# Optimization experiments

Measured on AMD Instinct MI355X. Metric: run time of the kernel, lower is better.

Reference implementation:

```python
import jax, jax.numpy as jnp
import numpy as np
import math

B, T, H, L, N = 8, 256, 1024, 6, 16
S = 3 * T          # interleaved (rtg, state, action) tokens
D = H // N
STATE_DIM, ACT_DIM, MAX_TSTEP, FF = 1024, 64, 4096, 4 * H
EPS = 1e-5


def _ln(x, g, b):
    m = jnp.mean(x, axis=-1, keepdims=True)
    v = jnp.var(x, axis=-1, keepdims=True)
    return (x - m) * jax.lax.rsqrt(v + EPS) * g + b


def setup_inputs() -> dict:
    key = jax.random.key(0)
    ks = jax.random.split(key, 32)
    sc = 0.02
    inp = {
        'timesteps': jax.random.randint(ks[0], (B, T), 0, MAX_TSTEP),
        'states': jax.random.randint(ks[1], (B, T), 0, STATE_DIM),
        'actions': jax.random.randint(ks[2], (B, T), 0, ACT_DIM),
        'returns_to_go': jax.random.normal(ks[3], (B, T, 1), jnp.float32),
        # embeddings
        'Wt': jax.random.normal(ks[4], (MAX_TSTEP, H), jnp.float32) * sc,
        'Ws': jax.random.normal(ks[5], (STATE_DIM, H), jnp.float32) * sc,
        'Wa': jax.random.normal(ks[6], (ACT_DIM, H), jnp.float32) * sc,
        'Wr': jax.random.normal(ks[7], (1, H), jnp.float32) * sc,
        'br': jnp.zeros((H,), jnp.float32),
        'lng': jnp.ones((H,), jnp.float32), 'lnb': jnp.zeros((H,), jnp.float32),
        # per-layer stacked params (weights stored [in,out]: y = x @ W + b)
        'Wq': jax.random.normal(ks[8], (L, H, H), jnp.float32) * sc,
        'bq': jnp.zeros((L, H), jnp.float32),
        'Wk': jax.random.normal(ks[9], (L, H, H), jnp.float32) * sc,
        'bk': jnp.zeros((L, H), jnp.float32),
        'Wv': jax.random.normal(ks[10], (L, H, H), jnp.float32) * sc,
        'bv': jnp.zeros((L, H), jnp.float32),
        'Wp': jax.random.normal(ks[11], (L, H, H), jnp.float32) * sc,
        'bp': jnp.zeros((L, H), jnp.float32),
        'W1': jax.random.normal(ks[12], (L, H, FF), jnp.float32) * sc,
        'b1': jnp.zeros((L, FF), jnp.float32),
        'W2': jax.random.normal(ks[13], (L, FF, H), jnp.float32) * sc,
        'b2': jnp.zeros((L, H), jnp.float32),
        'ln1g': jnp.ones((L, H), jnp.float32), 'ln1b': jnp.zeros((L, H), jnp.float32),
        'ln2g': jnp.ones((L, H), jnp.float32), 'ln2b': jnp.zeros((L, H), jnp.float32),
        # heads
        'Wrtg': jax.random.normal(ks[14], (H, 1), jnp.float32) * sc,
        'brtg': jnp.zeros((1,), jnp.float32),
        'Wst': jax.random.normal(ks[15], (H, STATE_DIM), jnp.float32) * sc,
        'bst': jnp.zeros((STATE_DIM,), jnp.float32),
        'Wac': jax.random.normal(ks[16], (H, ACT_DIM), jnp.float32) * sc,
        'bac': jnp.zeros((ACT_DIM,), jnp.float32),
    }
    return inp


def _attn(x, Wq, bq, Wk, bk, Wv, bv, Wp, bp, mask):
    q = (x @ Wq + bq).reshape(B, S, N, D)
    k = (x @ Wk + bk).reshape(B, S, N, D)
    v = (x @ Wv + bv).reshape(B, S, N, D)
    scores = jnp.einsum('bqhd,bkhd->bhqk', q, k) / math.sqrt(D)
    scores = jnp.where(mask, scores, -jnp.inf)
    p = jax.nn.softmax(scores, axis=-1)
    o = jnp.einsum('bhqk,bkhd->bqhd', p, v).reshape(B, S, H)
    return o @ Wp + bp


def _forward(timesteps, states, actions, returns_to_go, Wt, Ws, Wa, Wr, br,
             lng, lnb, Wq, bq, Wk, bk, Wv, bv, Wp, bp, W1, b1, W2, b2,
             ln1g, ln1b, ln2g, ln2b, Wrtg, brtg, Wst, bst, Wac, bac):
    te = Wt[timesteps]                         # [B,T,H]
    se = Ws[states] + te
    ae = Wa[actions] + te
    re = returns_to_go @ Wr + br + te
    # stack(dim=1).permute(0,2,1,3).reshape -> interleave (rtg, state, action)
    h = jnp.stack([re, se, ae], axis=2).reshape(B, S, H)
    h = _ln(h, lng, lnb)
    mask = jnp.tril(jnp.ones((S, S), bool))[None, None]
    for l in range(L):
        h = h + _attn(h, Wq[l], bq[l], Wk[l], bk[l], Wv[l], bv[l], Wp[l], bp[l], mask)
        h = _ln(h, ln1g[l], ln1b[l])
        h = h + (jax.nn.gelu(h @ W1[l] + b1[l], approximate=False) @ W2[l] + b2[l])
        h = _ln(h, ln2g[l], ln2b[l])
    h = h.reshape(B, 3, T, H)                  # as in the source (contiguous chunks)
    rtg_preds = h[:, 2] @ Wrtg + brtg
    state_preds = h[:, 2] @ Wst + bst
    action_preds = h[:, 1] @ Wac + bac         # discrete actions -> no tanh
    return (state_preds, action_preds, rtg_preds)


def reference(timesteps, states, actions, returns_to_go, Wt, Ws, Wa, Wr, br,
              lng, lnb, Wq, bq, Wk, bk, Wv, bv, Wp, bp, W1, b1, W2, b2,
              ln1g, ln1b, ln2g, ln2b, Wrtg, brtg, Wst, bst, Wac, bac):
    return _forward(timesteps, states, actions, returns_to_go, Wt, Ws, Wa, Wr, br,
                    lng, lnb, Wq, bq, Wk, bk, Wv, bv, Wp, bp, W1, b1, W2, b2,
                    ln1g, ln1b, ln2g, ln2b, Wrtg, brtg, Wst, bst, Wac, bac)
```

## Files before the change

### kernel.cpp

```cpp
#include <hip/hip_runtime.h>
#include <hip/hip_bf16.h>

#define DI __device__ __forceinline__

typedef unsigned short u16;
typedef __bf16 bf16x8 __attribute__((ext_vector_type(8)));
typedef unsigned short u16x8 __attribute__((ext_vector_type(8)));
typedef unsigned short u16x4 __attribute__((ext_vector_type(4)));
typedef float f32x4 __attribute__((ext_vector_type(4)));

static constexpr int Bb = 8, Tt = 256, Hh = 1024, Ll = 6, NHd = 16, Dh = 64;
static constexpr int Ss = 3 * Tt;
static constexpr int FFd = 4096;
static constexpr int BSr = Bb * Ss;
static constexpr int QKVld = 3072;

DI u16 f2bf(float f) {
  unsigned u = __builtin_bit_cast(unsigned, f);
  u += 0x7fffu + ((u >> 16) & 1u);
  return (u16)(u >> 16);
}

DI void gload_lds16(const u16* g, u16* l) {
  __builtin_amdgcn_global_load_lds((__attribute__((address_space(1))) void*)(g),
                                   (__attribute__((address_space(3))) void*)(l), 16, 0, 0);
}
DI bf16x8 ldl8(const u16* p) { return __builtin_bit_cast(bf16x8, *(const u16x8*)p); }
DI bf16x8 ldg8(const u16* p) { return __builtin_bit_cast(bf16x8, *(const u16x8*)p); }

DI void barRaw() {
  asm volatile("" ::: "memory");
  __builtin_amdgcn_s_barrier();
  asm volatile("" ::: "memory");
}

__global__ __launch_bounds__(256, 4) void gemm_db(
    const u16* __restrict__ A, const u16* __restrict__ Bt,
    const float* __restrict__ bias, const float* __restrict__ bias2,
    const float* __restrict__ bias3,
    float* __restrict__ outf, u16* __restrict__ outb,
    int Kstride, int Ksub, int ldc, int act, size_t psz)
{
  __shared__ u16 LA[3][128 * 32];
  __shared__ u16 LB[3][128 * 32];
  const int lane = threadIdx.x & 63, w = threadIdx.x >> 6;
  const int wr = w >> 1, wc = w & 1;
  const int l15 = lane & 15, l4 = lane >> 4;

  const int gx = gridDim.x, nwg = gx * gridDim.y;
  int f = blockIdx.y * gx + blockIdx.x;
  { int q = nwg >> 3, rr = nwg & 7, x = f & 7, idx = f >> 3;
    f = (x < rr ? x * (q + 1) : rr * (q + 1) + (x - rr) * q) + idx; }
  const int bm = f / gx, bn = f % gx;
  const int koff = blockIdx.z * Ksub;
  const int NT = Ksub >> 5;

  const int srow = lane >> 2;
  const int schunk = (((lane & 3) ^ ((srow >> 1) & 3)) << 3);
  unsigned aoff[2], boff[2];
#pragma unroll
  for (int i = 0; i < 2; ++i) {
    const int r = w * 32 + i * 16 + srow;
    aoff[i] = (unsigned)(bm * 128 + r) * (unsigned)Kstride + koff + schunk;
    boff[i] = (unsigned)(bn * 128 + r) * (unsigned)Kstride + koff + schunk;
  }

  auto stage = [&](int bsel, int kt) {
#pragma unroll
    for (int i = 0; i < 2; ++i) {
      gload_lds16(A + aoff[i] + kt * 32, &LA[bsel][(w * 32 + i * 16) * 32]);
      gload_lds16(Bt + boff[i] + kt * 32, &LB[bsel][(w * 32 + i * 16) * 32]);
    }
  };

  f32x4 acc[4][4] = {};

  stage(0, 0);
  stage(1, 1);
  asm volatile("s_waitcnt vmcnt(4)" ::: "memory");
  barRaw();

  const int ck = ((l4 ^ ((l15 >> 1) & 3)) << 3);
  int cur = 0;
  for (int t = 0; t < NT; ++t) {
    const int nxt = (cur + 2 >= 3) ? cur - 1 : cur + 2;
    if (t + 2 < NT) stage(nxt, t + 2);

    bf16x8 af[4], bf[4];
#pragma unroll
    for (int m = 0; m < 4; ++m)
      af[m] = ldl8(&LA[cur][(wr * 64 + m * 16 + l15) * 32 + ck]);
#pragma unroll
    for (int n = 0; n < 4; ++n)
      bf[n] = ldl8(&LB[cur][(wc * 64 + n * 16 + l15) * 32 + ck]);

    __builtin_amdgcn_s_setprio(1);
#pragma unroll
    for (int m = 0; m < 4; ++m)
#pragma unroll
      for (int n = 0; n < 4; ++n)
        acc[m][n] = __builtin_amdgcn_mfma_f32_16x16x32_bf16(af[m], bf[n], acc[m][n], 0, 0, 0);
    __builtin_amdgcn_s_setprio(0);

    if (t + 2 < NT)      asm volatile("s_waitcnt vmcnt(4)" ::: "memory");
    else if (t + 1 < NT) asm volatile("s_waitcnt vmcnt(0)" ::: "memory");
    barRaw();
    cur = (cur + 1 >= 3) ? 0 : cur + 1;
  }

#pragma unroll
  for (int n = 0; n < 4; ++n) {
    const int col = bn * 128 + wc * 64 + n * 16 + l15;
    float bval = 0.f;
    if (bias) {
      const float* bp_ = bias;
      int idx = col;
      if (bias2 && col >= 1024) { bp_ = (col >= 2048) ? bias3 : bias2; idx = col & 1023; }
      bval = bp_[idx];
    }
#pragma unroll
    for (int m = 0; m < 4; ++m) {
#pragma unroll
      for (int r = 0; r < 4; ++r) {
        const int row = bm * 128 + wr * 64 + m * 16 + l4 * 4 + r;
        float x = acc[m][n][r] + bval;
        if (act) x = 0.5f * x * (1.f + erff(x * 0.70710678118654752f));
        if (outf) outf[blockIdx.z * psz + (size_t)row * ldc + col] = x;
        if (outb) outb[(size_t)row * ldc + col] = f2bf(x);
      }
    }
  }
}

__global__ __launch_bounds__(256, 2) void gemm_bf16(
    const u16* __restrict__ A, const u16* __restrict__ Bt,
    const float* __restrict__ bias, float* __restrict__ outf,
    int M, int N, int K, int ldc, int Nstore, int rowmode, int rowoff)
{
  __shared__ u16 As[128 * 64];
  __shared__ u16 Bs[128 * 64];
  const int tid = threadIdx.x;
  const int lane = tid & 63;
  const int w = tid >> 6;
  const int wr = w >> 1, wc = w & 1;
  const int bn = blockIdx.x, bm = blockIdx.y;
  const int l3 = lane >> 3, l7 = lane & 7, l15 = lane & 15, l4 = lane >> 4;

  f32x4 acc[4][4] = {};

  const int schunk = (l7 ^ l3) << 3;
  size_t aoff[4], boff[4];
#pragma unroll
  for (int i = 0; i < 4; ++i) {
    int r = bm * 128 + w * 32 + i * 8 + l3;
    int ar = rowmode ? ((r >> 8) * Ss + rowoff + (r & 255)) : r;
    aoff[i] = (size_t)ar * K + schunk;
    boff[i] = (size_t)(bn * 128 + w * 32 + i * 8 + l3) * K + schunk;
  }

  for (int kt = 0; kt < K; kt += 64) {
    __syncthreads();
#pragma unroll
    for (int i = 0; i < 4; ++i) {
      gload_lds16(A + aoff[i] + kt, &As[(w * 32 + i * 8) * 64]);
      gload_lds16(Bt + boff[i] + kt, &Bs[(w * 32 + i * 8) * 64]);
    }
    __syncthreads();

    bf16x8 af[4][2], bf[4][2];
#pragma unroll
    for (int m = 0; m < 4; ++m) {
#pragma unroll
      for (int kk = 0; kk < 2; ++kk) {
        const int slot = ((kk * 4 + l4) ^ l7) << 3;
        af[m][kk] = ldl8(&As[(wr * 64 + m * 16 + l15) * 64 + slot]);
        bf[m][kk] = ldl8(&Bs[(wc * 64 + m * 16 + l15) * 64 + slot]);
      }
    }
#pragma unroll
    for (int m = 0; m < 4; ++m)
#pragma unroll
      for (int n = 0; n < 4; ++n)
#pragma unroll
        for (int kk = 0; kk < 2; ++kk)
          acc[m][n] = __builtin_amdgcn_mfma_f32_16x16x32_bf16(af[m][kk], bf[n][kk], acc[m][n], 0, 0, 0);
  }

#pragma unroll
  for (int n = 0; n < 4; ++n) {
    const int col = bn * 128 + wc * 64 + n * 16 + l15;
    const bool cok = col < Nstore;
    const float bv = (cok && bias) ? bias[col] : 0.f;
#pragma unroll
    for (int m = 0; m < 4; ++m) {
#pragma unroll
      for (int r = 0; r < 4; ++r) {
        const int row = bm * 128 + wr * 64 + m * 16 + l4 * 4 + r;
        if (cok) outf[(size_t)row * ldc + col] = acc[m][n][r] + bv;
      }
    }
  }
}

__global__ __launch_bounds__(256, 3) void attn_flash(
    const u16* __restrict__ qkv, const u16* __restrict__ vt, u16* __restrict__ o)
{
  __shared__ u16 Kl[2][64 * 64];
  __shared__ u16 Vl[2][64 * 64];
  __shared__ u16 Pl[4][16 * 64];
  const int qt = blockIdx.x, h = blockIdx.y, b = blockIdx.z;
  const int lane = threadIdx.x & 63, w = threadIdx.x >> 6;
  const int l15 = lane & 15, l4 = lane >> 4;

  const size_t qoff = (size_t)(b * Ss + qt * 64 + w * 16 + l15) * QKVld + h * Dh + l4 * 8;
  const bf16x8 aq0 = ldg8(qkv + qoff), aq1 = ldg8(qkv + qoff + 32);

  const u16* kg = qkv + (size_t)b * Ss * QKVld + 1024 + h * Dh;
  const u16* vg = vt + (size_t)(b * NHd + h) * Dh * Ss;

  int srow[2], scs[2];
#pragma unroll
  for (int i = 0; i < 2; ++i) {
    srow[i] = (w * 2 + i) * 8 + (lane >> 3);
    scs[i] = ((lane & 7) ^ (srow[i] & 7)) * 8;
  }

  float m[4] = {-1e30f, -1e30f, -1e30f, -1e30f};
  float lsum[4] = {0.f, 0.f, 0.f, 0.f};
  f32x4 oa[4] = {};

  auto stage = [&](int bsel, int kb) {
#pragma unroll
    for (int i = 0; i < 2; ++i) {
      gload_lds16(kg + (size_t)(kb * 64 + srow[i]) * QKVld + scs[i], &Kl[bsel][(w * 2 + i) * 8 * 64]);
      gload_lds16(vg + (size_t)srow[i] * Ss + kb * 64 + scs[i], &Vl[bsel][(w * 2 + i) * 8 * 64]);
    }
  };

  stage(0, 0);
  __syncthreads();
  int buf = 0;
  for (int kb = 0; kb <= qt; ++kb) {
    if (kb < qt) stage(buf ^ 1, kb + 1);

    f32x4 sc[4];
    __builtin_amdgcn_s_setprio(1);
#pragma unroll
    for (int fj = 0; fj < 4; ++fj) {
      const u16* kp = &Kl[buf][(fj * 16 + l15) * 64];
      const int r7 = l15 & 7;
      bf16x8 kf0 = ldl8(kp + ((l4 ^ r7) << 3));
      bf16x8 kf1 = ldl8(kp + (((4 + l4) ^ r7) << 3));
      f32x4 zz = {};
      zz = __builtin_amdgcn_mfma_f32_16x16x32_bf16(aq0, kf0, zz, 0, 0, 0);
      sc[fj] = __builtin_amdgcn_mfma_f32_16x16x32_bf16(aq1, kf1, zz, 0, 0, 0);
    }
    __builtin_amdgcn_s_setprio(0);

    float pm[4] = {-1e30f, -1e30f, -1e30f, -1e30f};
    const bool diag = (kb == qt);
#pragma unroll
    for (int fj = 0; fj < 4; ++fj)
#pragma unroll
      for (int r = 0; r < 4; ++r) {
        float s = sc[fj][r] * 0.125f;
        if (diag && (fj * 16 + l15) > (w * 16 + l4 * 4 + r)) s = -1e30f;
        sc[fj][r] = s;
        pm[r] = fmaxf(pm[r], s);
      }
#pragma unroll
    for (int d = 1; d < 16; d <<= 1)
#pragma unroll
      for (int r = 0; r < 4; ++r) pm[r] = fmaxf(pm[r], __shfl_xor(pm[r], d));

    float al[4], ps[4];
#pragma unroll
    for (int r = 0; r < 4; ++r) {
      float mn = fmaxf(m[r], pm[r]);
      al[r] = __expf(m[r] - mn);
      m[r] = mn;
      ps[r] = 0.f;
    }
#pragma unroll
    for (int fj = 0; fj < 4; ++fj)
#pragma unroll
      for (int r = 0; r < 4; ++r) {
        float p = __expf(sc[fj][r] - m[r]);
        sc[fj][r] = p;
        ps[r] += p;
      }
#pragma unroll
    for (int d = 1; d < 16; d <<= 1)
#pragma unroll
      for (int r = 0; r < 4; ++r) ps[r] += __shfl_xor(ps[r], d);
#pragma unroll
    for (int r = 0; r < 4; ++r) lsum[r] = lsum[r] * al[r] + ps[r];
#pragma unroll
    for (int fn = 0; fn < 4; ++fn)
#pragma unroll
      for (int r = 0; r < 4; ++r) oa[fn][r] *= al[r];

#pragma unroll
    for (int fj = 0; fj < 4; ++fj)
#pragma unroll
      for (int r = 0; r < 4; ++r) {
        const int key = fj * 16 + l15, qloc = l4 * 4 + r;
        Pl[w][qloc * 64 + (((key >> 3) ^ (qloc & 7)) << 3) + (key & 7)] = f2bf(sc[fj][r]);
      }

    const int q7 = l15 & 7;
    bf16x8 pa0 = ldl8(&Pl[w][l15 * 64 + ((l4 ^ q7) << 3)]);
    bf16x8 pa1 = ldl8(&Pl[w][l15 * 64 + (((4 + l4) ^ q7) << 3)]);
    __builtin_amdgcn_s_setprio(1);
#pragma unroll
    for (int fn = 0; fn < 4; ++fn) {
      const u16* vp = &Vl[buf][(fn * 16 + l15) * 64];
      bf16x8 vf0 = ldl8(vp + ((l4 ^ q7) << 3));
      bf16x8 vf1 = ldl8(vp + (((4 + l4) ^ q7) << 3));
      oa[fn] = __builtin_amdgcn_mfma_f32_16x16x32_bf16(pa0, vf0, oa[fn], 0, 0, 0);
      oa[fn] = __builtin_amdgcn_mfma_f32_16x16x32_bf16(pa1, vf1, oa[fn], 0, 0, 0);
    }
    __builtin_amdgcn_s_setprio(0);
    __syncthreads();
    buf ^= 1;
  }

#pragma unroll
  for (int fn = 0; fn < 4; ++fn)
#pragma unroll
    for (int r = 0; r < 4; ++r) {
      const int row = b * Ss + qt * 64 + w * 16 + l4 * 4 + r;
      o[(size_t)row * Hh + h * Dh + fn * 16 + l15] = f2bf(oa[fn][r] / lsum[r]);
    }
}

__global__ __launch_bounds__(256) void embed_ln(
    const int* __restrict__ timesteps, const int* __restrict__ states,
    const int* __restrict__ actions, const float* __restrict__ rtg,
    const float* __restrict__ Wt, const float* __restrict__ Ws,
    const float* __restrict__ Wa, const float* __restrict__ Wr,
    const float* __restrict__ br, const float* __restrict__ lng,
    const float* __restrict__ lnb, float* __restrict__ hout, u16* __restrict__ xb)
{
  __shared__ float red[8];
  const int s = blockIdx.x;
  const int b = s / Ss, sl = s % Ss;
  const int tt = sl / 3, kind = sl % 3;
  const int bt = b * Tt + tt;
  const int e = threadIdx.x * 4;

  const float4 tv = *(const float4*)(Wt + (size_t)timesteps[bt] * Hh + e);
  float v[4];
  if (kind == 0) {
    const float rr = rtg[bt];
    const float4 w4 = *(const float4*)(Wr + e);
    const float4 b4 = *(const float4*)(br + e);
    v[0] = rr * w4.x + b4.x + tv.x; v[1] = rr * w4.y + b4.y + tv.y;
    v[2] = rr * w4.z + b4.z + tv.z; v[3] = rr * w4.w + b4.w + tv.w;
  } else {
    const float* emb = (kind == 1) ? (Ws + (size_t)states[bt] * Hh)
                                   : (Wa + (size_t)actions[bt] * Hh);
    const float4 e4 = *(const float4*)(emb + e);
    v[0] = e4.x + tv.x; v[1] = e4.y + tv.y; v[2] = e4.z + tv.z; v[3] = e4.w + tv.w;
  }
  float s1 = v[0] + v[1] + v[2] + v[3];
  float s2 = v[0]*v[0] + v[1]*v[1] + v[2]*v[2] + v[3]*v[3];
#pragma unroll
  for (int d = 32; d; d >>= 1) { s1 += __shfl_xor(s1, d); s2 += __shfl_xor(s2, d); }
  if ((threadIdx.x & 63) == 0) { red[threadIdx.x >> 6] = s1; red[4 + (threadIdx.x >> 6)] = s2; }
  __syncthreads();
  s1 = red[0] + red[1] + red[2] + red[3];
  s2 = red[4] + red[5] + red[6] + red[7];
  const float mean = s1 * (1.f / 1024.f);
  const float var = s2 * (1.f / 1024.f) - mean * mean;
  const float rs = rsqrtf(var + 1e-5f);
  const float4 g4 = *(const float4*)(lng + e);
  const float4 bb4 = *(const float4*)(lnb + e);
  float o0 = (v[0] - mean) * rs * g4.x + bb4.x;
  float o1 = (v[1] - mean) * rs * g4.y + bb4.y;
  float o2 = (v[2] - mean) * rs * g4.z + bb4.z;
  float o3 = (v[3] - mean) * rs * g4.w + bb4.w;
  *(float4*)(hout + (size_t)s * Hh + e) = make_float4(o0, o1, o2, o3);
  u16x4 ov = {f2bf(o0), f2bf(o1), f2bf(o2), f2bf(o3)};
  *(u16x4*)(xb + (size_t)s * Hh + e) = ov;
}

__global__ __launch_bounds__(256) void ln_kernel(
    const float* __restrict__ inA, const float* __restrict__ inB,
    const float* __restrict__ resid, const float* __restrict__ bias,
    const float* __restrict__ g, const float* __restrict__ bta,
    float* __restrict__ hout, u16* __restrict__ xb)
{
  __shared__ float red[8];
  const int row = blockIdx.x;
  const int e = threadIdx.x * 4;
  const float4 a4 = *(const float4*)(inA + (size_t)row * Hh + e);
  float v[4] = {a4.x, a4.y, a4.z, a4.w};
  if (inB) {
    const float4 b4 = *(const float4*)(inB + (size_t)row * Hh + e);
    v[0] += b4.x; v[1] += b4.y; v[2] += b4.z; v[3] += b4.w;
  }
  if (resid) {
    const float4 r4 = *(const float4*)(resid + (size_t)row * Hh + e);
    v[0] += r4.x; v[1] += r4.y; v[2] += r4.z; v[3] += r4.w;
  }
  if (bias) {
    const float4 c4 = *(const float4*)(bias + e);
    v[0] += c4.x; v[1] += c4.y; v[2] += c4.z; v[3] += c4.w;
  }
  float s1 = v[0] + v[1] + v[2] + v[3];
  float s2 = v[0]*v[0] + v[1]*v[1] + v[2]*v[2] + v[3]*v[3];
#pragma unroll
  for (int d = 32; d; d >>= 1) { s1 += __shfl_xor(s1, d); s2 += __shfl_xor(s2, d); }
  if ((threadIdx.x & 63) == 0) { red[threadIdx.x >> 6] = s1; red[4 + (threadIdx.x >> 6)] = s2; }
  __syncthreads();
  s1 = red[0] + red[1] + red[2] + red[3];
  s2 = red[4] + red[5] + red[6] + red[7];
  const float mean = s1 * (1.f / 1024.f);
  const float var = s2 * (1.f / 1024.f) - mean * mean;
  const float rs = rsqrtf(var + 1e-5f);
  const float4 g4 = *(const float4*)(g + e);
  const float4 b4 = *(const float4*)(bta + e);
  float o0 = (v[0] - mean) * rs * g4.x + b4.x;
  float o1 = (v[1] - mean) * rs * g4.y + b4.y;
  float o2 = (v[2] - mean) * rs * g4.z + b4.z;
  float o3 = (v[3] - mean) * rs * g4.w + b4.w;
  *(float4*)(hout + (size_t)row * Hh + e) = make_float4(o0, o1, o2, o3);
  u16x4 ov = {f2bf(o0), f2bf(o1), f2bf(o2), f2bf(o3)};
  *(u16x4*)(xb + (size_t)row * Hh + e) = ov;
}

__global__ __launch_bounds__(256) void transpose_w(
    const float* __restrict__ W, u16* __restrict__ Wt, int Kd, int Nd, int Nout)
{
  __shared__ float tile[32][33];
  const int k0 = blockIdx.x * 32, n0 = blockIdx.y * 32;
  const int tx = threadIdx.x & 31, ty = threadIdx.x >> 5;
#pragma unroll
  for (int rr = 0; rr < 4; ++rr) {
    const int kk = ty + rr * 8;
    const int n = n0 + tx;
    tile[kk][tx] = (n < Nd) ? W[(size_t)(k0 + kk) * Nd + n] : 0.f;
  }
  __syncthreads();
#pragma unroll
  for (int rr = 0; rr < 4; ++rr) {
    Wt[(size_t)(n0 + ty + rr * 8) * Kd + k0 + tx] = f2bf(tile[tx][ty + rr * 8]);
  }
}

__global__ __launch_bounds__(256) void transpose_v(
    const u16* __restrict__ v, u16* __restrict__ vt)
{
  __shared__ u16 tile[64][72];
  const int s0 = blockIdx.x * 64, h = blockIdx.y, b = blockIdx.z;
  const int j8 = (threadIdx.x & 7) * 8;
#pragma unroll
  for (int half = 0; half < 2; ++half) {
    const int i = (threadIdx.x >> 3) + half * 32;
    *(u16x8*)&tile[i][j8] =
        *(const u16x8*)&v[(size_t)(b * Ss + s0 + i) * QKVld + 2048 + h * 64 + j8];
  }
  __syncthreads();
#pragma unroll
  for (int half = 0; half < 2; ++half) {
    const int d = (threadIdx.x >> 3) + half * 32;
    u16x8 ov;
#pragma unroll
    for (int ee = 0; ee < 8; ++ee) ov[ee] = tile[j8 + ee][d];
    *(u16x8*)&vt[((size_t)(b * NHd + h) * 64 + d) * Ss + s0 + j8] = ov;
  }
}

__global__ __launch_bounds__(256) void rtg_head(
    const float* __restrict__ h, const float* __restrict__ Wr1,
    const float* __restrict__ br1, float* __restrict__ out)
{
  const int lane = threadIdx.x & 63, w = threadIdx.x >> 6;
  const int row = blockIdx.x * 4 + w;
  const int b = row >> 8, tt = row & 255;
  const float* x = h + (size_t)(b * Ss + 512 + tt) * Hh;
  float s = 0.f;
  for (int e = lane; e < Hh; e += 64) s += x[e] * Wr1[e];
#pragma unroll
  for (int d = 32; d; d >>= 1) s += __shfl_xor(s, d);
  if (lane == 0) out[row] = s + br1[0];
}

extern "C" void kernel_launch(void* const* d_in, const int* in_sizes, int n_in,
                              void* d_out, int out_size, void* d_ws, size_t ws_size,
                              hipStream_t stream)
{
  (void)in_sizes; (void)n_in; (void)out_size; (void)ws_size;
  const int*   timesteps = (const int*)d_in[0];
  const int*   states    = (const int*)d_in[1];
  const int*   actions   = (const int*)d_in[2];
  const float* rtg       = (const float*)d_in[3];
  const float* Wt   = (const float*)d_in[4];
  const float* Ws   = (const float*)d_in[5];
  const float* Wa   = (const float*)d_in[6];
  const float* Wr   = (const float*)d_in[7];
  const float* br   = (const float*)d_in[8];
  const float* lng  = (const float*)d_in[9];
  const float* lnb  = (const float*)d_in[10];
  const float* Wq   = (const float*)d_in[11];
  const float* bq   = (const float*)d_in[12];
  const float* Wk   = (const float*)d_in[13];
  const float* bk   = (const float*)d_in[14];
  const float* Wv   = (const float*)d_in[15];
  const float* bv   = (const float*)d_in[16];
  const float* Wp   = (const float*)d_in[17];
  const float* bp   = (const float*)d_in[18];
  const float* W1   = (const float*)d_in[19];
  const float* b1   = (const float*)d_in[20];
  const float* W2   = (const float*)d_in[21];
  const float* b2   = (const float*)d_in[22];
  const float* ln1g = (const float*)d_in[23];
  const float* ln1b = (const float*)d_in[24];
  const float* ln2g = (const float*)d_in[25];
  const float* ln2b = (const float*)d_in[26];
  const float* Wrtg = (const float*)d_in[27];
  const float* brtg = (const float*)d_in[28];
  const float* Wst  = (const float*)d_in[29];
  const float* bst  = (const float*)d_in[30];
  const float* Wac  = (const float*)d_in[31];
  const float* bac  = (const float*)d_in[32];

  char* wp = (char*)d_ws;
  auto alloc = [&](size_t bytes) { void* p = wp; wp += (bytes + 511) & ~(size_t)511; return p; };
  float* hbuf = (float*)alloc((size_t)BSr * Hh * 4);
  float* p0   = (float*)alloc((size_t)BSr * Hh * 4);
  float* p1   = (float*)alloc((size_t)BSr * Hh * 4);
  u16* xb   = (u16*)alloc((size_t)BSr * Hh * 2);
  u16* qkvb = (u16*)alloc((size_t)BSr * QKVld * 2);
  u16* vtb  = (u16*)alloc((size_t)BSr * Hh * 2);
  u16* ob   = (u16*)alloc((size_t)BSr * Hh * 2);
  u16* ub   = (u16*)alloc((size_t)BSr * FFd * 2);
  u16* W3T  = (u16*)alloc((size_t)3 * Hh * Hh * 2);
  u16* WpT  = (u16*)alloc((size_t)Hh * Hh * 2);
  u16* W1T  = (u16*)alloc((size_t)FFd * Hh * 2);
  u16* W2T  = (u16*)alloc((size_t)Hh * FFd * 2);
  u16* WstT = (u16*)alloc((size_t)Hh * Hh * 2);
  u16* WacT = (u16*)alloc((size_t)128 * Hh * 2);

  float* out_state = (float*)d_out;
  float* out_act   = out_state + (size_t)2048 * 1024;
  float* out_rtg   = out_act + (size_t)2048 * 64;

  const size_t PSZ = (size_t)BSr * Hh;

  transpose_w<<<dim3(32, 32, 1), 256, 0, stream>>>(Wst, WstT, 1024, 1024, 1024);
  transpose_w<<<dim3(32, 4, 1), 256, 0, stream>>>(Wac, WacT, 1024, 64, 128);
  embed_ln<<<BSr, 256, 0, stream>>>(timesteps, states, actions, rtg, Wt, Ws, Wa, Wr,
                                    br, lng, lnb, hbuf, xb);

  for (int l = 0; l < Ll; ++l) {
    transpose_w<<<dim3(32, 32, 1), 256, 0, stream>>>(Wq + (size_t)l * Hh * Hh, W3T, 1024, 1024, 1024);
    transpose_w<<<dim3(32, 32, 1), 256, 0, stream>>>(Wk + (size_t)l * Hh * Hh, W3T + (size_t)Hh * Hh, 1024, 1024, 1024);
    transpose_w<<<dim3(32, 32, 1), 256, 0, stream>>>(Wv + (size_t)l * Hh * Hh, W3T + (size_t)2 * Hh * Hh, 1024, 1024, 1024);
    transpose_w<<<dim3(32, 32, 1), 256, 0, stream>>>(Wp + (size_t)l * Hh * Hh, WpT, 1024, 1024, 1024);
    transpose_w<<<dim3(32, 128, 1), 256, 0, stream>>>(W1 + (size_t)l * Hh * FFd, W1T, 1024, 4096, 4096);
    transpose_w<<<dim3(128, 32, 1), 256, 0, stream>>>(W2 + (size_t)l * FFd * Hh, W2T, 4096, 1024, 1024);

    gemm_db<<<dim3(24, 48, 1), 256, 0, stream>>>(
        xb, W3T, bq + l * Hh, bk + l * Hh, bv + l * Hh, nullptr, qkvb,
        Hh, Hh, QKVld, 0, 0);
    transpose_v<<<dim3(12, 16, 8), 256, 0, stream>>>(qkvb, vtb);
    attn_flash<<<dim3(12, 16, 8), 256, 0, stream>>>(qkvb, vtb, ob);
    gemm_db<<<dim3(8, 48, 2), 256, 0, stream>>>(
        ob, WpT, nullptr, nullptr, nullptr, p0, nullptr,
        Hh, 512, Hh, 0, PSZ);
    ln_kernel<<<BSr, 256, 0, stream>>>(p0, p1, hbuf, bp + l * Hh,
                                       ln1g + l * Hh, ln1b + l * Hh, hbuf, xb);
    gemm_db<<<dim3(32, 48, 1), 256, 0, stream>>>(
        xb, W1T, b1 + l * FFd, nullptr, nullptr, nullptr, ub,
        Hh, Hh, FFd, 1, 0);
    gemm_db<<<dim3(8, 48, 2), 256, 0, stream>>>(
        ub, W2T, nullptr, nullptr, nullptr, p0, nullptr,
        FFd, 2048, Hh, 0, PSZ);
    ln_kernel<<<BSr, 256, 0, stream>>>(p0, p1, hbuf, b2 + l * Hh,
                                       ln2g + l * Hh, ln2b + l * Hh, hbuf, xb);
  }

  gemm_bf16<<<dim3(8, 16), 256, 0, stream>>>(xb, WstT, bst, out_state,
                                             2048, 1024, 1024, 1024, 1024, 1, 512);
  gemm_bf16<<<dim3(1, 16), 256, 0, stream>>>(xb, WacT, bac, out_act,
                                             2048, 128, 1024, 64, 64, 1, 256);
  rtg_head<<<512, 256, 0, stream>>>(hbuf, Wrtg, brtg, out_rtg);
}
```

Before: 2.311 ms.

## Enlarge GEMM tile to 128x256 with BK=64 and 8 waves

Replaces the 128x128x32 4-wave GEMM with a 128x256x64 tile using 512 threads (8 waves), a single triple-buffered LDS array and a new XOR swizzle over 8 chunks. Each wave still computes a 64x64 output, but twice as many K-steps go into each barrier interval and the A tile is reused across more columns. The aim is to cut global/LDS traffic per FLOP and the number of barriers. In exchange it uses far more LDS (about 144KB per block), which lowers occupancy, and it halves the grid size, so fewer workgroups are available to fill the CUs.

```diff
diff --git a/kernel.cpp b/kernel.cpp
--- a/kernel.cpp
+++ b/kernel.cpp
@@ -34,17 +34,16 @@
   asm volatile("" ::: "memory");
 }
 
-__global__ __launch_bounds__(256, 4) void gemm_db(
+__global__ __launch_bounds__(512, 2) void gemm_big(
     const u16* __restrict__ A, const u16* __restrict__ Bt,
     const float* __restrict__ bias, const float* __restrict__ bias2,
     const float* __restrict__ bias3,
     float* __restrict__ outf, u16* __restrict__ outb,
     int Kstride, int Ksub, int ldc, int act, size_t psz)
 {
-  __shared__ u16 LA[3][128 * 32];
-  __shared__ u16 LB[3][128 * 32];
+  __shared__ u16 L[3][384 * 64];
   const int lane = threadIdx.x & 63, w = threadIdx.x >> 6;
-  const int wr = w >> 1, wc = w & 1;
+  const int wr = w >> 2, wc = w & 3;
   const int l15 = lane & 15, l4 = lane >> 4;
 
   const int gx = gridDim.x, nwg = gx * gridDim.y;
@@ -53,56 +52,65 @@
     f = (x < rr ? x * (q + 1) : rr * (q + 1) + (x - rr) * q) + idx; }
   const int bm = f / gx, bn = f % gx;
   const int koff = blockIdx.z * Ksub;
-  const int NT = Ksub >> 5;
-
-  const int srow = lane >> 2;
-  const int schunk = (((lane & 3) ^ ((srow >> 1) & 3)) << 3);
-  unsigned aoff[2], boff[2];
-#pragma unroll
-  for (int i = 0; i < 2; ++i) {
-    const int r = w * 32 + i * 16 + srow;
-    aoff[i] = (unsigned)(bm * 128 + r) * (unsigned)Kstride + koff + schunk;
-    boff[i] = (unsigned)(bn * 128 + r) * (unsigned)Kstride + koff + schunk;
-  }
+  const int NT = Ksub >> 6;
+
+  const int srow = lane >> 3;
+  const int schunk = ((lane & 7) ^ srow) << 3;
+  size_t aoff[2], boff[4];
+#pragma unroll
+  for (int j = 0; j < 2; ++j)
+    aoff[j] = (size_t)(bm * 128 + j * 64 + w * 8 + srow) * Kstride + koff + schunk;
+#pragma unroll
+  for (int j = 0; j < 4; ++j)
+    boff[j] = (size_t)(bn * 256 + j * 64 + w * 8 + srow) * Kstride + koff + schunk;
 
   auto stage = [&](int bsel, int kt) {
 #pragma unroll
-    for (int i = 0; i < 2; ++i) {
-      gload_lds16(A + aoff[i] + kt * 32, &LA[bsel][(w * 32 + i * 16) * 32]);
-      gload_lds16(Bt + boff[i] + kt * 32, &LB[bsel][(w * 32 + i * 16) * 32]);
-    }
+    for (int j = 0; j < 2; ++j)
+      gload_lds16(A + aoff[j] + kt * 64, &L[bsel][j * 4096 + w * 512]);
+#pragma unroll
+    for (int j = 0; j < 4; ++j)
+      gload_lds16(Bt + boff[j] + kt * 64, &L[bsel][8192 + j * 4096 + w * 512]);
   };
 
   f32x4 acc[4][4] = {};
 
   stage(0, 0);
   stage(1, 1);
-  asm volatile("s_waitcnt vmcnt(4)" ::: "memory");
+  asm volatile("s_waitcnt vmcnt(6)" ::: "memory");
   barRaw();
 
-  const int ck = ((l4 ^ ((l15 >> 1) & 3)) << 3);
+  const int ckb = l15 & 7;
   int cur = 0;
   for (int t = 0; t < NT; ++t) {
     const int nxt = (cur + 2 >= 3) ? cur - 1 : cur + 2;
     if (t + 2 < NT) stage(nxt, t + 2);
 
-    bf16x8 af[4], bf[4];
+    bf16x8 af[4][2], bf[4][2];
 #pragma unroll
     for (int m = 0; m < 4; ++m)
-      af[m] = ldl8(&LA[cur][(wr * 64 + m * 16 + l15) * 32 + ck]);
+#pragma unroll
+      for (int kk = 0; kk < 2; ++kk)
+        af[m][kk] = ldl8(&L[cur][(wr * 64 + m * 16 + l15) * 64 +
+                                 (((kk * 4 + l4) ^ ckb) << 3)]);
 #pragma unroll
     for (int n = 0; n < 4; ++n)
-      bf[n] = ldl8(&LB[cur][(wc * 64 + n * 16 + l15) * 32 + ck]);
+#pragma unroll
+      for (int kk = 0; kk < 2; ++kk)
+        bf[n][kk] = ldl8(&L[cur][(128 + wc * 64 + n * 16 + l15) * 64 +
+                                 (((kk * 4 + l4) ^ ckb) << 3)]);
 
     __builtin_amdgcn_s_setprio(1);
 #pragma unroll
     for (int m = 0; m < 4; ++m)
 #pragma unroll
       for (int n = 0; n < 4; ++n)
-        acc[m][n] = __builtin_amdgcn_mfma_f32_16x16x32_bf16(af[m], bf[n], acc[m][n], 0, 0, 0);
+#pragma unroll
+        for (int kk = 0; kk < 2; ++kk)
+          acc[m][n] = __builtin_amdgcn_mfma_f32_16x16x32_bf16(af[m][kk], bf[n][kk], acc[m][n], 0, 0, 0);
     __builtin_amdgcn_s_setprio(0);
 
-    if (t + 2 < NT)      asm volatile("s_waitcnt vmcnt(4)" ::: "memory");
+    if (t + 2 < NT)      asm volatile("s_waitcnt vmcnt(6)" ::: "memory");
     else if (t + 1 < NT) asm volatile("s_waitcnt vmcnt(0)" ::: "memory");
     barRaw();
     cur = (cur + 1 >= 3) ? 0 : cur + 1;
@@ -110,7 +118,7 @@
 
 #pragma unroll
   for (int n = 0; n < 4; ++n) {
-    const int col = bn * 128 + wc * 64 + n * 16 + l15;
+    const int col = bn * 256 + wc * 64 + n * 16 + l15;
     float bval = 0.f;
     if (bias) {
       const float* bp_ = bias;
@@ -562,20 +570,20 @@
     transpose_w<<<dim3(32, 128, 1), 256, 0, stream>>>(W1 + (size_t)l * Hh * FFd, W1T, 1024, 4096, 4096);
     transpose_w<<<dim3(128, 32, 1), 256, 0, stream>>>(W2 + (size_t)l * FFd * Hh, W2T, 4096, 1024, 1024);
 
-    gemm_db<<<dim3(24, 48, 1), 256, 0, stream>>>(
+    gemm_big<<<dim3(12, 48, 1), 512, 0, stream>>>(
         xb, W3T, bq + l * Hh, bk + l * Hh, bv + l * Hh, nullptr, qkvb,
         Hh, Hh, QKVld, 0, 0);
     transpose_v<<<dim3(12, 16, 8), 256, 0, stream>>>(qkvb, vtb);
     attn_flash<<<dim3(12, 16, 8), 256, 0, stream>>>(qkvb, vtb, ob);
-    gemm_db<<<dim3(8, 48, 2), 256, 0, stream>>>(
+    gemm_big<<<dim3(4, 48, 2), 512, 0, stream>>>(
         ob, WpT, nullptr, nullptr, nullptr, p0, nullptr,
         Hh, 512, Hh, 0, PSZ);
     ln_kernel<<<BSr, 256, 0, stream>>>(p0, p1, hbuf, bp + l * Hh,
                                        ln1g + l * Hh, ln1b + l * Hh, hbuf, xb);
-    gemm_db<<<dim3(32, 48, 1), 256, 0, stream>>>(
+    gemm_big<<<dim3(16, 48, 1), 512, 0, stream>>>(
         xb, W1T, b1 + l * FFd, nullptr, nullptr, nullptr, ub,
         Hh, Hh, FFd, 1, 0);
-    gemm_db<<<dim3(8, 48, 2), 256, 0, stream>>>(
+    gemm_big<<<dim3(4, 48, 2), 512, 0, stream>>>(
         ub, W2T, nullptr, nullptr, nullptr, p0, nullptr,
         FFd, 2048, Hh, 0, PSZ);
     ln_kernel<<<BSr, 256, 0, stream>>>(p0, p1, hbuf, b2 + l * Hh,
```

New measurement: 2.479 ms. 1.07x slower.

## Stage GEMM epilogue through LDS for coalesced row-wise global stores

Applied to the files above, without the earlier changes.

Merges the A/B LDS buffers into one flat shared array and reuses it after the main loop to stage the output tile. Rows are then written to global memory contiguously (bf16 pairs or float2) instead of scattered 2-byte/4-byte column-strided stores from the MFMA layout. The fp32 path stages in two halves to fit in LDS. Launch bounds drop to 3 waves per SIMD to allow the larger LDS footprint, which adds barriers and may reduce occupancy.

```diff
diff --git a/kernel.cpp b/kernel.cpp
--- a/kernel.cpp
+++ b/kernel.cpp
@@ -34,15 +34,14 @@
   asm volatile("" ::: "memory");
 }
 
-__global__ __launch_bounds__(256, 4) void gemm_db(
+__global__ __launch_bounds__(256, 3) void gemm_db(
     const u16* __restrict__ A, const u16* __restrict__ Bt,
     const float* __restrict__ bias, const float* __restrict__ bias2,
     const float* __restrict__ bias3,
     float* __restrict__ outf, u16* __restrict__ outb,
     int Kstride, int Ksub, int ldc, int act, size_t psz)
 {
-  __shared__ u16 LA[3][128 * 32];
-  __shared__ u16 LB[3][128 * 32];
+  __shared__ u16 SM[24576];
   const int lane = threadIdx.x & 63, w = threadIdx.x >> 6;
   const int wr = w >> 1, wc = w & 1;
   const int l15 = lane & 15, l4 = lane >> 4;
@@ -68,8 +67,8 @@
   auto stage = [&](int bsel, int kt) {
 #pragma unroll
     for (int i = 0; i < 2; ++i) {
-      gload_lds16(A + aoff[i] + kt * 32, &LA[bsel][(w * 32 + i * 16) * 32]);
-      gload_lds16(Bt + boff[i] + kt * 32, &LB[bsel][(w * 32 + i * 16) * 32]);
+      gload_lds16(A + aoff[i] + kt * 32, &SM[bsel * 4096 + (w * 32 + i * 16) * 32]);
+      gload_lds16(Bt + boff[i] + kt * 32, &SM[12288 + bsel * 4096 + (w * 32 + i * 16) * 32]);
     }
   };
 
@@ -89,10 +88,10 @@
     bf16x8 af[4], bf[4];
 #pragma unroll
     for (int m = 0; m < 4; ++m)
-      af[m] = ldl8(&LA[cur][(wr * 64 + m * 16 + l15) * 32 + ck]);
+      af[m] = ldl8(&SM[cur * 4096 + (wr * 64 + m * 16 + l15) * 32 + ck]);
 #pragma unroll
     for (int n = 0; n < 4; ++n)
-      bf[n] = ldl8(&LB[cur][(wc * 64 + n * 16 + l15) * 32 + ck]);
+      bf[n] = ldl8(&SM[12288 + cur * 4096 + (wc * 64 + n * 16 + l15) * 32 + ck]);
 
     __builtin_amdgcn_s_setprio(1);
 #pragma unroll
@@ -108,25 +107,71 @@
     cur = (cur + 1 >= 3) ? 0 : cur + 1;
   }
 
-#pragma unroll
-  for (int n = 0; n < 4; ++n) {
-    const int col = bn * 128 + wc * 64 + n * 16 + l15;
-    float bval = 0.f;
-    if (bias) {
-      const float* bp_ = bias;
-      int idx = col;
-      if (bias2 && col >= 1024) { bp_ = (col >= 2048) ? bias3 : bias2; idx = col & 1023; }
-      bval = bp_[idx];
-    }
-#pragma unroll
-    for (int m = 0; m < 4; ++m) {
-#pragma unroll
-      for (int r = 0; r < 4; ++r) {
-        const int row = bm * 128 + wr * 64 + m * 16 + l4 * 4 + r;
-        float x = acc[m][n][r] + bval;
-        if (act) x = 0.5f * x * (1.f + erff(x * 0.70710678118654752f));
-        if (outf) outf[blockIdx.z * psz + (size_t)row * ldc + col] = x;
-        if (outb) outb[(size_t)row * ldc + col] = f2bf(x);
+  if (outb) {
+#pragma unroll
+    for (int n = 0; n < 4; ++n) {
+      const int col = wc * 64 + n * 16 + l15;
+      const int gcol = bn * 128 + col;
+      float bval = 0.f;
+      if (bias) {
+        const float* bp_ = bias;
+        int idx = gcol;
+        if (bias2 && gcol >= 1024) { bp_ = (gcol >= 2048) ? bias3 : bias2; idx = gcol & 1023; }
+        bval = bp_[idx];
+      }
+#pragma unroll
+      for (int m = 0; m < 4; ++m) {
+#pragma unroll
+        for (int r = 0; r < 4; ++r) {
+          const int lrow = wr * 64 + m * 16 + l4 * 4 + r;
+          float x = acc[m][n][r] + bval;
+          if (act) x = 0.5f * x * (1.f + erff(x * 0.70710678118654752f));
+          SM[lrow * 128 + col] = f2bf(x);
+        }
+      }
+    }
+    barRaw();
+#pragma unroll 4
+    for (int rr = 0; rr < 32; ++rr) {
+      const int row = rr * 4 + w;
+      *(unsigned*)&outb[(size_t)(bm * 128 + row) * ldc + bn * 128 + lane * 2] =
+          *(const unsigned*)&SM[row * 128 + lane * 2];
+    }
+  } else if (outf) {
+    float* Cf = (float*)SM;
+#pragma unroll
+    for (int half = 0; half < 2; ++half) {
+      barRaw();
+      if (wr == half) {
+#pragma unroll
+        for (int n = 0; n < 4; ++n) {
+          const int col = wc * 64 + n * 16 + l15;
+          const int gcol = bn * 128 + col;
+          float bval = 0.f;
+          if (bias) {
+            const float* bp_ = bias;
+            int idx = gcol;
+            if (bias2 && gcol >= 1024) { bp_ = (gcol >= 2048) ? bias3 : bias2; idx = gcol & 1023; }
+            bval = bp_[idx];
+          }
+#pragma unroll
+          for (int m = 0; m < 4; ++m) {
+#pragma unroll
+            for (int r = 0; r < 4; ++r) {
+              float x = acc[m][n][r] + bval;
+              if (act) x = 0.5f * x * (1.f + erff(x * 0.70710678118654752f));
+              Cf[(m * 16 + l4 * 4 + r) * 128 + col] = x;
+            }
+          }
+        }
+      }
+      barRaw();
+#pragma unroll 4
+      for (int rr = 0; rr < 16; ++rr) {
+        const int row = rr * 4 + w;
+        *(float2*)&outf[blockIdx.z * psz +
+                        (size_t)(bm * 128 + half * 64 + row) * ldc + bn * 128 + lane * 2] =
+            *(const float2*)&Cf[row * 128 + lane * 2];
       }
     }
   }
```

New measurement: 2.264 ms. 1.02x faster.
